# Kernel optimization log

Measured on AMD Instinct MI355X. Metric: run time of the kernel, lower is better.

Reference implementation:

```python
import jax, jax.numpy as jnp
import numpy as np

N = 50000      # nodes
E = 800000     # edges (avg degree 16)
G = 128        # g_dim (input feature dim)
H1 = 128       # h1_dim (RGCN output dim)
H2 = 32        # h2_dim (per-head channels)
HEADS = 4
R = 6          # num_relations
OUT = H2 * HEADS  # 128, BatchNorm width
BN_EPS = 1e-5


def setup_inputs() -> dict:
    key = jax.random.key(0)
    k = jax.random.split(key, 16)
    s = 0.05
    return {
        "node_features": jax.random.normal(k[0], (N, G), jnp.float32),
        "node_type": jax.random.randint(k[1], (N,), 0, 3),
        "edge_index": jax.random.randint(k[2], (2, E), 0, N),
        "edge_type": jax.random.randint(k[3], (E,), 0, R),
        # RGCNConv params (root_weight=True, bias=True, aggr='mean')
        "W_rel": jax.random.normal(k[4], (R, G, H1), jnp.float32) * s,
        "W_root": jax.random.normal(k[5], (G, H1), jnp.float32) * s,
        "b_rgcn": jnp.zeros((H1,), jnp.float32),
        # TransformerConv params (concat=True, root_weight=True via lin_skip)
        "Wq": jax.random.normal(k[6], (H1, OUT), jnp.float32) * s,
        "bq": jnp.zeros((OUT,), jnp.float32),
        "Wk": jax.random.normal(k[7], (H1, OUT), jnp.float32) * s,
        "bk": jnp.zeros((OUT,), jnp.float32),
        "Wv": jax.random.normal(k[8], (H1, OUT), jnp.float32) * s,
        "bv": jnp.zeros((OUT,), jnp.float32),
        "Wskip": jax.random.normal(k[9], (H1, OUT), jnp.float32) * s,
        "bskip": jnp.zeros((OUT,), jnp.float32),
        # BatchNorm1d affine params
        "bn_gamma": jnp.ones((OUT,), jnp.float32),
        "bn_beta": jnp.zeros((OUT,), jnp.float32),
    }


def _gnn_forward(node_features, edge_index, edge_type,
                 W_rel, W_root, b_rgcn,
                 Wq, bq, Wk, bk, Wv, bv, Wskip, bskip,
                 bn_gamma, bn_beta):
    src, dst = edge_index[0], edge_index[1]  # message flows src (j) -> dst (i)

    # ---- RGCNConv with mean aggregation per relation ----
    # Transform all nodes under every relation: [R, N, H1]
    xt = jnp.einsum('nd,rdo->rno', node_features, W_rel)
    msg = xt[edge_type, src]                          # [E, H1]
    seg = edge_type * N + dst                         # composite (relation, dst) segment id
    agg = jax.ops.segment_sum(msg, seg, num_segments=R * N).reshape(R, N, H1)
    cnt = jax.ops.segment_sum(jnp.ones((E,), msg.dtype), seg,
                              num_segments=R * N).reshape(R, N)
    x = node_features @ W_root + b_rgcn + (agg / jnp.maximum(cnt, 1.0)[:, :, None]).sum(0)

    # ---- TransformerConv (heads=HEADS, concat=True) ----
    q = (x @ Wq + bq).reshape(N, HEADS, H2)
    kk = (x @ Wk + bk).reshape(N, HEADS, H2)
    v = (x @ Wv + bv).reshape(N, HEADS, H2)

    score = (q[dst] * kk[src]).sum(-1) / np.sqrt(H2)  # [E, HEADS]
    m = jax.ops.segment_max(score, dst, num_segments=N)   # -inf for isolated nodes
    m = jnp.where(jnp.isfinite(m), m, 0.0)
    ex = jnp.exp(score - m[dst])
    den = jax.ops.segment_sum(ex, dst, num_segments=N)
    alpha = ex / (den[dst] + 1e-16)                   # [E, HEADS]

    out = jax.ops.segment_sum(alpha[:, :, None] * v[src], dst,
                              num_segments=N).reshape(N, OUT)
    out = out + x @ Wskip + bskip                     # skip / root connection

    # ---- BatchNorm1d (training-mode batch stats) + LeakyReLU(0.01) ----
    mu = out.mean(0)
    var = out.var(0)  # biased, as torch uses for normalization
    y = (out - mu) * jax.lax.rsqrt(var + BN_EPS) * bn_gamma + bn_beta
    return jax.nn.leaky_relu(y, negative_slope=0.01)


def reference(node_features, node_type, edge_index, edge_type,
              W_rel, W_root, b_rgcn,
              Wq, bq, Wk, bk, Wv, bv, Wskip, bskip,
              bn_gamma, bn_beta):
    # node_type is accepted but unused, matching the original forward.
    return _gnn_forward(node_features, edge_index, edge_type,
                        W_rel, W_root, b_rgcn,
                        Wq, bq, Wk, bk, Wv, bv, Wskip, bskip,
                        bn_gamma, bn_beta)
```

## Files before the change

### kernel.cpp

```cpp
#include <hip/hip_runtime.h>
#include <hip/hip_fp16.h>
#include <stdint.h>

#define G      128
#define OUTW   128
#define RNUM   6

typedef unsigned short us;
typedef _Float16 f16x8 __attribute__((ext_vector_type(8)));
typedef float    f32x4 __attribute__((ext_vector_type(4)));

__device__ inline float h2f(us u) { __half h; *(us*)&h = u; return __half2float(h); }
__device__ inline us f2h(float f) { __half h = __float2half(f); return *(us*)&h; }

union FragU { f16x8 v; ushort4 u[2]; };

__global__ void count_kernel(const int* __restrict__ ei, const int* __restrict__ et,
                             int* __restrict__ segcnt, int N, int E) {
    int e = blockIdx.x * blockDim.x + threadIdx.x;
    if (e >= E) return;
    int dst = ei[E + e];
    int r   = et[e];
    atomicAdd(&segcnt[dst * RNUM + r], 1);
}

__global__ __launch_bounds__(256)
void scan_part(const int* __restrict__ cnt, int* __restrict__ bsum, int n) {
    __shared__ int s[256];
    int base = blockIdx.x * 1024, t = threadIdx.x;
    int v = 0;
    for (int j = 0; j < 4; ++j) { int idx = base + j * 256 + t; if (idx < n) v += cnt[idx]; }
    s[t] = v; __syncthreads();
    for (int off = 128; off; off >>= 1) { if (t < off) s[t] += s[t + off]; __syncthreads(); }
    if (!t) bsum[blockIdx.x] = s[0];
}

__global__ __launch_bounds__(512)
void scan_top(const int* __restrict__ bsum, int* __restrict__ boff,
              int* __restrict__ segptr, int nb, int n) {
    __shared__ int s[512];
    int t = threadIdx.x;
    int v = (t < nb) ? bsum[t] : 0;
    s[t] = v;
    __syncthreads();
    for (int off = 1; off < 512; off <<= 1) {
        int y = (t >= off) ? s[t - off] : 0;
        __syncthreads();
        s[t] += y;
        __syncthreads();
    }
    if (t < nb) boff[t + 1] = s[t];
    if (!t) boff[0] = 0;
    if (t == nb - 1) segptr[n] = s[t];
}

__global__ __launch_bounds__(256)
void scan_apply(const int* __restrict__ cnt, const int* __restrict__ boff,
                int* __restrict__ segptr, int* __restrict__ cursor, int n) {
    __shared__ int L[1024];
    __shared__ int SS[256];
    int base = blockIdx.x * 1024, t = threadIdx.x;
    for (int j = 0; j < 4; ++j) { int idx = base + j * 256 + t; L[j * 256 + t] = (idx < n) ? cnt[idx] : 0; }
    __syncthreads();
    int s0 = L[t*4] + L[t*4+1] + L[t*4+2] + L[t*4+3];
    SS[t] = s0; __syncthreads();
    for (int off = 1; off < 256; off <<= 1) {
        int y = (t >= off) ? SS[t - off] : 0;
        __syncthreads();
        SS[t] += y;
        __syncthreads();
    }
    int e0 = (t ? SS[t - 1] : 0) + boff[blockIdx.x];
    int4 ov;
    int a;
    a = L[t*4+0]; ov.x = e0; e0 += a;
    a = L[t*4+1]; ov.y = e0; e0 += a;
    a = L[t*4+2]; ov.z = e0; e0 += a;
    a = L[t*4+3]; ov.w = e0; e0 += a;
    int idx0 = base + t * 4;
    if (idx0 + 3 < n) {
        *(int4*)(segptr + idx0) = ov;
        *(int4*)(cursor + idx0) = ov;
    } else {
        int vals[4] = {ov.x, ov.y, ov.z, ov.w};
        for (int k = 0; k < 4; ++k)
            if (idx0 + k < n) { segptr[idx0 + k] = vals[k]; cursor[idx0 + k] = vals[k]; }
    }
}

__global__ void scatter_kernel(const int* __restrict__ ei, const int* __restrict__ et,
                               int* __restrict__ cursor, unsigned* __restrict__ esrc,
                               int N, int E) {
    int e = blockIdx.x * blockDim.x + threadIdx.x;
    if (e >= E) return;
    int src = ei[e];
    int dst = ei[E + e];
    int r   = et[e];
    int pos = atomicAdd(&cursor[dst * RNUM + r], 1);
    esrc[pos] = (unsigned)src;
}

__global__ __launch_bounds__(256)
void prep_kernel(const float* __restrict__ x, us* __restrict__ xh,
                 const float* __restrict__ Wrel, const float* __restrict__ Wroot,
                 ushort4* __restrict__ Btr,
                 const float* __restrict__ Wq, const float* __restrict__ Wk,
                 const float* __restrict__ Wv, const float* __restrict__ Ws,
                 ushort4* __restrict__ Btq, int xblocks) {
    int b = blockIdx.x;
    if (b < xblocks) {
        int i = b * 256 + threadIdx.x;
        float4 a = ((const float4*)x)[2*i];
        float4 c = ((const float4*)x)[2*i+1];
        ushort4 u0 = { f2h(a.x), f2h(a.y), f2h(a.z), f2h(a.w) };
        ushort4 u1 = { f2h(c.x), f2h(c.y), f2h(c.z), f2h(c.w) };
        ((ushort4*)xh)[2*i]   = u0;
        ((ushort4*)xh)[2*i+1] = u1;
    } else if (b < xblocks + 112) {
        int idx = (b - xblocks) * 256 + threadIdx.x;
        int kq = idx >> 7, n = idx & 127;
        ushort4 o;
        us* op = (us*)&o;
#pragma unroll
        for (int i = 0; i < 4; ++i) {
            int k = 4 * kq + i;
            float v = (k < 768) ? Wrel[(size_t)k * 128 + n] : Wroot[(size_t)(k - 768) * 128 + n];
            op[i] = f2h(v);
        }
        Btr[idx] = o;
    } else {
        int idx = (b - xblocks - 112) * 256 + threadIdx.x;
        int kq = idx >> 9, n = idx & 511;
        int quad = n >> 7, nl = n & 127;
        const float* W = (quad == 0) ? Wq : (quad == 1) ? Wk : (quad == 2) ? Wv : Ws;
        ushort4 o;
        us* op = (us*)&o;
#pragma unroll
        for (int i = 0; i < 4; ++i) {
            int k = 4 * kq + i;
            op[i] = f2h(W[(size_t)k * 128 + nl]);
        }
        Btq[idx] = o;
    }
}

__global__ __launch_bounds__(256)
void agg_kernel(const us* __restrict__ xh, const int* __restrict__ segptr,
                const unsigned* __restrict__ esrc, us* __restrict__ meanF, int N) {
    const int wv = threadIdx.x >> 6, l = threadIdx.x & 63;
    const int i = blockIdx.x * 4 + wv;
    if (i >= N) return;
    const int t = i >> 4, row = i & 15;
    const int e0 = __builtin_amdgcn_readfirstlane(segptr[i * RNUM]);
    const int e1 = __builtin_amdgcn_readfirstlane(segptr[i * RNUM + RNUM]);

    int rcur = 0;
    int sstart = e0;
    int bnext = __builtin_amdgcn_readfirstlane(segptr[i * RNUM + 1]);
    float2 a = {0.f, 0.f};
    us* wbase = meanF + (size_t)t * 12288 + row * 4 + (l & 1) * 2;
    const int kqo = (l >> 1) * 64;

#define FLUSH() { \
    float sc_ = 1.f / fmaxf((float)(bnext - sstart), 1.f); \
    ushort2 t2_ = { f2h(a.x * sc_), f2h(a.y * sc_) }; \
    *(ushort2*)(wbase + rcur * 2048 + kqo) = t2_; \
    a.x = 0.f; a.y = 0.f; \
    sstart = bnext; ++rcur; \
    if (rcur < RNUM) bnext = __builtin_amdgcn_readfirstlane(segptr[i * RNUM + rcur + 1]); }

#define GET(J) ((unsigned)__shfl((int)pv, (J)))
#define LX(Q)  (*(const ushort2*)(xh + (size_t)(Q) * G + 2 * l))
#define STEP(U) { while (p >= bnext && rcur < RNUM - 1) FLUSH(); \
                  a.x += h2f((U).x); a.y += h2f((U).y); ++p; }

    int p = e0;
    for (int wb = e0; wb < e1; wb += 64) {
        const int nc = min(64, e1 - wb);
        unsigned pv = (wb + l < e1) ? esrc[wb + l] : 0u;
        int j = 0;
        while (j + 8 <= nc) {
            unsigned q0 = GET(j+0), q1 = GET(j+1), q2 = GET(j+2), q3 = GET(j+3);
            unsigned q4 = GET(j+4), q5 = GET(j+5), q6 = GET(j+6), q7 = GET(j+7);
            ushort2 u0 = LX(q0), u1 = LX(q1), u2 = LX(q2), u3 = LX(q3);
            ushort2 u4 = LX(q4), u5 = LX(q5), u6 = LX(q6), u7 = LX(q7);
            STEP(u0); STEP(u1); STEP(u2); STEP(u3);
            STEP(u4); STEP(u5); STEP(u6); STEP(u7);
            j += 8;
        }
        while (j + 2 <= nc) {
            unsigned q0 = GET(j), q1 = GET(j+1);
            ushort2 u0 = LX(q0), u1 = LX(q1);
            STEP(u0); STEP(u1);
            j += 2;
        }
        if (j < nc) {
            unsigned q0 = GET(j);
            ushort2 u0 = LX(q0);
            STEP(u0);
            ++j;
        }
    }
    while (rcur < RNUM) FLUSH();
#undef STEP
#undef LX
#undef GET
#undef FLUSH
}

__global__ __launch_bounds__(256)
void rgcn_mfma2(const us* __restrict__ xh, const us* __restrict__ meanF,
                const ushort4* __restrict__ Btr, const float* __restrict__ brg,
                us* __restrict__ xrh, int N) {
    const int tid = threadIdx.x;
    const int w = tid >> 6, l = tid & 63;
    const int lh = l >> 4, lm = l & 15;
    const int base = blockIdx.x * 64;
    const int ntile = N >> 4;
    const int t  = min(blockIdx.x * 4 + w, ntile - 1);
    const int gr = min(base + w * 16 + lm, N - 1);
    const us* amean = meanF + (size_t)t * 12288 + lm * 4;
    const us* aroot = xh + (size_t)gr * 128;

    f32x4 acc[8];
#pragma unroll
    for (int ct = 0; ct < 8; ++ct) {
        float b = brg[ct * 16 + lm];
        acc[ct] = (f32x4){b, b, b, b};
    }

#pragma unroll
    for (int s = 0; s < 28; ++s) {
        const int kqg = s * 8 + lh;
        FragU af;
        if (s < 24) {
            af.u[0] = *(const ushort4*)(amean + kqg * 64);
            af.u[1] = *(const ushort4*)(amean + (kqg + 4) * 64);
        } else {
            const int kql = kqg - 192;
            af.u[0] = *(const ushort4*)(aroot + kql * 4);
            af.u[1] = *(const ushort4*)(aroot + kql * 4 + 16);
        }
        const ushort4* B0 = Btr + (size_t)kqg * 128 + lm;
        const ushort4* B1 = B0 + 4 * 128;
#pragma unroll
        for (int ct = 0; ct < 8; ++ct) {
            FragU bf;
            bf.u[0] = B0[ct * 16];
            bf.u[1] = B1[ct * 16];
            acc[ct] = __builtin_amdgcn_mfma_f32_16x16x32_f16(af.v, bf.v, acc[ct], 0, 0, 0);
        }
    }

#pragma unroll
    for (int ct = 0; ct < 8; ++ct) {
#pragma unroll
        for (int i = 0; i < 4; ++i) {
            int r = base + w * 16 + 4 * lh + i;
            if (r < N) xrh[(size_t)r * 128 + ct * 16 + lm] = f2h(acc[ct][i]);
        }
    }
}

__global__ __launch_bounds__(512)
void qkvs_mfma2(const us* __restrict__ xrh, const ushort4* __restrict__ Btq,
                const float* __restrict__ bq, const float* __restrict__ bk,
                const float* __restrict__ bv, const float* __restrict__ bs,
                float* __restrict__ qs, us* __restrict__ kvh, int N) {
    const int tid = threadIdx.x;
    const int w = tid >> 6, l = tid & 63;
    const int quad = w & 3, tp = w >> 2;
    const int lh = l >> 4, lm = l & 15;
    const int base = blockIdx.x * 64;
    const float* bias = (quad == 0) ? bq : (quad == 1) ? bk : (quad == 2) ? bv : bs;

#pragma unroll
    for (int tt = 0; tt < 2; ++tt) {
        const int tile = tp * 2 + tt;
        const int ar = min(base + tile * 16 + lm, N - 1);
        const us* ap = xrh + (size_t)ar * 128;
        f32x4 acc[8];
#pragma unroll
        for (int ct = 0; ct < 8; ++ct) {
            float b = bias[ct * 16 + lm];
            acc[ct] = (f32x4){b, b, b, b};
        }
#pragma unroll
        for (int s = 0; s < 4; ++s) {
            const int kq = s * 8 + lh;
            FragU af;
            af.u[0] = *(const ushort4*)(ap + kq * 4);
            af.u[1] = *(const ushort4*)(ap + kq * 4 + 16);
            const ushort4* B0 = Btq + (size_t)kq * 512 + quad * 128 + lm;
            const ushort4* B1 = B0 + 4 * 512;
#pragma unroll
            for (int ct = 0; ct < 8; ++ct) {
                FragU bf;
                bf.u[0] = B0[ct * 16];
                bf.u[1] = B1[ct * 16];
                acc[ct] = __builtin_amdgcn_mfma_f32_16x16x32_f16(af.v, bf.v, acc[ct], 0, 0, 0);
            }
        }
        if (quad == 0 || quad == 3) {
            int off = (quad == 0) ? 0 : 128;
#pragma unroll
            for (int ct = 0; ct < 8; ++ct)
#pragma unroll
                for (int i = 0; i < 4; ++i) {
                    int r = base + tile * 16 + 4 * lh + i;
                    if (r < N) qs[(size_t)r * 256 + off + ct * 16 + lm] = acc[ct][i];
                }
        } else {
            int off = (quad == 1) ? 0 : 2;
#pragma unroll
            for (int ct = 0; ct < 8; ++ct)
#pragma unroll
                for (int i = 0; i < 4; ++i) {
                    int r = base + tile * 16 + 4 * lh + i;
                    int col = ct * 16 + lm;
                    if (r < N) kvh[(size_t)r * 256 + (col >> 1) * 4 + (col & 1) + off] = f2h(acc[ct][i]);
                }
        }
    }
}

__global__ __launch_bounds__(256)
void attn_kernel(const float* __restrict__ qs, const us* __restrict__ kvh,
                 const int* __restrict__ segptr, const unsigned* __restrict__ esrc,
                 float* __restrict__ out, float* __restrict__ bnS,
                 float* __restrict__ bnQ, int N) {
    __shared__ float sS[128], sQ[128];
    const int tid = threadIdx.x;
    if (tid < 128) { sS[tid] = 0.f; sQ[tid] = 0.f; }
    __syncthreads();

    const int wv = tid >> 6, l = tid & 63;
    const int stride = gridDim.x * 4;
    const float QS = 0.17677669529663687f;
    float2 bsum = {0.f, 0.f}, bsq = {0.f, 0.f};

    for (int i = blockIdx.x * 4 + wv; i < N; i += stride) {
        float2 q2 = *(const float2*)(qs + (size_t)i * 256 + 2*l);
        q2.x *= QS; q2.y *= QS;

        float m = -INFINITY, den = 0.f;
        float2 acc = {0.f, 0.f};
        const int e0 = segptr[(size_t)i * RNUM], e1 = segptr[(size_t)i * RNUM + RNUM];

#define KVLOAD(P) (*(const ushort4*)(kvh + (size_t)(P) * 256 + 4*l))
#define SCORE(U, S) { \
    float s_ = q2.x * h2f((U).x) + q2.y * h2f((U).y); \
    s_ += __shfl_xor(s_, 1, 16); s_ += __shfl_xor(s_, 2, 16); \
    s_ += __shfl_xor(s_, 4, 16); s_ += __shfl_xor(s_, 8, 16); \
    S = s_; }

        for (int base = e0; base < e1; base += 64) {
            const int nc = min(64, e1 - base);
            unsigned pv = 0;
            if (base + l < e1) pv = esrc[base + l];
            int j = 0;
            for (; j + 4 <= nc; j += 4) {
                unsigned p0 = (unsigned)__shfl((int)pv, j+0);
                unsigned p1 = (unsigned)__shfl((int)pv, j+1);
                unsigned p2 = (unsigned)__shfl((int)pv, j+2);
                unsigned p3 = (unsigned)__shfl((int)pv, j+3);
                ushort4 k0 = KVLOAD(p0), k1 = KVLOAD(p1), k2 = KVLOAD(p2), k3 = KVLOAD(p3);
                float s0, s1, s2, s3;
                SCORE(k0, s0); SCORE(k1, s1); SCORE(k2, s2); SCORE(k3, s3);
                float mx = fmaxf(fmaxf(fmaxf(s0, s1), fmaxf(s2, s3)), m);
                float rs = __expf(m - mx);
                float p0e = __expf(s0 - mx), p1e = __expf(s1 - mx);
                float p2e = __expf(s2 - mx), p3e = __expf(s3 - mx);
                den = den * rs + ((p0e + p1e) + (p2e + p3e));
                acc.x = acc.x * rs + p0e*h2f(k0.z) + p1e*h2f(k1.z) + p2e*h2f(k2.z) + p3e*h2f(k3.z);
                acc.y = acc.y * rs + p0e*h2f(k0.w) + p1e*h2f(k1.w) + p2e*h2f(k2.w) + p3e*h2f(k3.w);
                m = mx;
            }
            for (; j < nc; ++j) {
                unsigned p0 = (unsigned)__shfl((int)pv, j);
                ushort4 k0 = KVLOAD(p0);
                float s0; SCORE(k0, s0);
                float mx = fmaxf(m, s0);
                float rs = __expf(m - mx);
                float pe = __expf(s0 - mx);
                den = den * rs + pe;
                acc.x = acc.x * rs + pe * h2f(k0.z);
                acc.y = acc.y * rs + pe * h2f(k0.w);
                m = mx;
            }
        }
#undef SCORE
#undef KVLOAD

        float inv = 1.f / (den + 1e-16f);
        float2 sk = *(const float2*)(qs + (size_t)i * 256 + 128 + 2*l);
        float2 o = { acc.x * inv + sk.x, acc.y * inv + sk.y };
        *(float2*)(out + (size_t)i * OUTW + 2*l) = o;
        bsum.x += o.x; bsum.y += o.y;
        bsq.x  += o.x * o.x; bsq.y += o.y * o.y;
    }

    atomicAdd(&sS[2*l],     bsum.x);
    atomicAdd(&sS[2*l + 1], bsum.y);
    atomicAdd(&sQ[2*l],     bsq.x);
    atomicAdd(&sQ[2*l + 1], bsq.y);
    __syncthreads();
    if (tid < 128) {
        atomicAdd(&bnS[tid], sS[tid]);
        atomicAdd(&bnQ[tid], sQ[tid]);
    }
}

__global__ __launch_bounds__(256)
void apply_kernel(float* __restrict__ out, const float* __restrict__ bnS,
                  const float* __restrict__ bnQ, const float* __restrict__ gamma,
                  const float* __restrict__ beta, int N, int total4) {
    __shared__ float A_s[128], B_s[128];
    const int tid = threadIdx.x;
    if (tid < 128) {
        float fN  = (float)N;
        float mu  = bnS[tid] / fN;
        float var = bnQ[tid] / fN - mu * mu;
        float rv  = rsqrtf(var + 1e-5f);
        float A   = rv * gamma[tid];
        A_s[tid] = A;
        B_s[tid] = beta[tid] - mu * A;
    }
    __syncthreads();
    for (int idx4 = blockIdx.x * 256 + tid; idx4 < total4; idx4 += gridDim.x * 256) {
        float4 v = ((const float4*)out)[idx4];
        int c0 = (idx4 * 4) & 127;
        float y;
        y = A_s[c0    ] * v.x + B_s[c0    ]; v.x = (y > 0.f) ? y : 0.01f * y;
        y = A_s[c0 + 1] * v.y + B_s[c0 + 1]; v.y = (y > 0.f) ? y : 0.01f * y;
        y = A_s[c0 + 2] * v.z + B_s[c0 + 2]; v.z = (y > 0.f) ? y : 0.01f * y;
        y = A_s[c0 + 3] * v.w + B_s[c0 + 3]; v.w = (y > 0.f) ? y : 0.01f * y;
        ((float4*)out)[idx4] = v;
    }
}

static inline char* alignp(char* p) {
    return (char*)(((uintptr_t)p + 255) & ~(uintptr_t)255);
}

extern "C" void kernel_launch(void* const* d_in, const int* in_sizes, int n_in,
                              void* d_out, int out_size, void* d_ws, size_t ws_size,
                              hipStream_t stream) {
    const float* x     = (const float*)d_in[0];
    const int*   ei    = (const int*)  d_in[2];
    const int*   et    = (const int*)  d_in[3];
    const float* Wrel  = (const float*)d_in[4];
    const float* Wroot = (const float*)d_in[5];
    const float* brg   = (const float*)d_in[6];
    const float* Wq    = (const float*)d_in[7];
    const float* bq    = (const float*)d_in[8];
    const float* Wk    = (const float*)d_in[9];
    const float* bk    = (const float*)d_in[10];
    const float* Wv    = (const float*)d_in[11];
    const float* bv    = (const float*)d_in[12];
    const float* Wsk   = (const float*)d_in[13];
    const float* bsk   = (const float*)d_in[14];
    const float* gamma = (const float*)d_in[15];
    const float* beta  = (const float*)d_in[16];
    float* out = (float*)d_out;

    const int N = in_sizes[0] / G;
    const int E = in_sizes[3];
    const int NSEG = N * RNUM;
    const int NB_SCAN = (NSEG + 1023) / 1024;

    char* w = (char*)d_ws;
    int* segcnt = (int*)w;           w += (size_t)NSEG * 4;
    float* bnS = (float*)w;          w += 128 * 4;
    float* bnQ = (float*)w;          w += 128 * 4;
    size_t zero_bytes = (size_t)(w - (char*)d_ws);
    w = alignp(w);
    int* bsum  = (int*)w;            w += 512 * 4;
    int* boff  = (int*)w;            w += 513 * 4;
    w = alignp(w);
    int* segptr = (int*)w;           w += (size_t)(NSEG + 1) * 4;
    w = alignp(w);
    int* cursor = (int*)w;           w += (size_t)NSEG * 4;
    w = alignp(w);
    unsigned* esrc = (unsigned*)w;   w += (size_t)E * 4;
    w = alignp(w);
    us* xh     = (us*)w;             w += (size_t)N * G * 2;
    w = alignp(w);
    us* xrh    = (us*)w;             w += (size_t)N * OUTW * 2;
    w = alignp(w);
    ushort4* Btr = (ushort4*)w;      w += (size_t)224 * 128 * 8;
    w = alignp(w);
    ushort4* Btq = (ushort4*)w;      w += (size_t)32 * 512 * 8;
    w = alignp(w);
    us*    meanF = (us*)w;
    float* qs    = (float*)w;
    us*    kvh   = (us*)(w + (size_t)N * 256 * 4);

    hipMemsetAsync(d_ws, 0, zero_bytes, stream);

    int eb = (E + 255) / 256;
    count_kernel<<<eb, 256, 0, stream>>>(ei, et, segcnt, N, E);

    scan_part<<<NB_SCAN, 256, 0, stream>>>(segcnt, bsum, NSEG);
    scan_top<<<1, 512, 0, stream>>>(bsum, boff, segptr, NB_SCAN, NSEG);
    scan_apply<<<NB_SCAN, 256, 0, stream>>>(segcnt, boff, segptr, cursor, NSEG);

    scatter_kernel<<<eb, 256, 0, stream>>>(ei, et, cursor, esrc, N, E);

    int xblocks = N * G / 8 / 256;
    prep_kernel<<<xblocks + 112 + 64, 256, 0, stream>>>(x, xh, Wrel, Wroot, Btr,
                                                        Wq, Wk, Wv, Wsk, Btq, xblocks);

    agg_kernel<<<(N + 3) / 4, 256, 0, stream>>>(xh, segptr, esrc, meanF, N);

    rgcn_mfma2<<<(N + 63) / 64, 256, 0, stream>>>(xh, meanF, Btr, brg, xrh, N);

    qkvs_mfma2<<<(N + 63) / 64, 512, 0, stream>>>(xrh, Btq, bq, bk, bv, bsk, qs, kvh, N);

    attn_kernel<<<2048, 256, 0, stream>>>(qs, kvh, segptr, esrc, out, bnS, bnQ, N);

    int total4 = N * OUTW / 4;
    apply_kernel<<<2048, 256, 0, stream>>>(out, bnS, bnQ, gamma, beta, N, total4);
}
```

Before: 500.8 us.

## Reuse weight fragments across two row tiles, store Q/skip in fp16, half-wave attention

The RGCN and QKVS MFMA kernels now have each wave compute two 16-row tiles, so every weight fragment loaded from global memory feeds twice as many MFMAs. Q and skip outputs are stored as fp16 instead of fp32, halving that intermediate's traffic and shrinking the workspace. The attention kernel now handles two destination nodes per wave, one per 32-lane half, with 16-byte K/V loads and 4 channels per lane. This raises register pressure and adds fp16 rounding of Q and skip values.

```diff
diff --git a/kernel.cpp b/kernel.cpp
--- a/kernel.cpp
+++ b/kernel.cpp
@@ -12,6 +12,7 @@
 
 __device__ inline float h2f(us u) { __half h; *(us*)&h = u; return __half2float(h); }
 __device__ inline us f2h(float f) { __half h = __float2half(f); return *(us*)&h; }
+__device__ inline float2 h22(int u) { return __half22float2(*(__half2*)&u); }
 
 union FragU { f16x8 v; ushort4 u[2]; };
 
@@ -209,123 +210,156 @@
 }
 
 __global__ __launch_bounds__(256)
-void rgcn_mfma2(const us* __restrict__ xh, const us* __restrict__ meanF,
+void rgcn_mfma3(const us* __restrict__ xh, const us* __restrict__ meanF,
                 const ushort4* __restrict__ Btr, const float* __restrict__ brg,
                 us* __restrict__ xrh, int N) {
     const int tid = threadIdx.x;
     const int w = tid >> 6, l = tid & 63;
     const int lh = l >> 4, lm = l & 15;
-    const int base = blockIdx.x * 64;
+    const int rowbase = blockIdx.x * 128 + w * 32;
     const int ntile = N >> 4;
-    const int t  = min(blockIdx.x * 4 + w, ntile - 1);
-    const int gr = min(base + w * 16 + lm, N - 1);
-    const us* amean = meanF + (size_t)t * 12288 + lm * 4;
-    const us* aroot = xh + (size_t)gr * 128;
-
-    f32x4 acc[8];
-#pragma unroll
-    for (int ct = 0; ct < 8; ++ct) {
-        float b = brg[ct * 16 + lm];
-        acc[ct] = (f32x4){b, b, b, b};
-    }
-
-#pragma unroll
-    for (int s = 0; s < 28; ++s) {
+
+    const us* amean[2];
+    const us* aroot[2];
+#pragma unroll
+    for (int tt = 0; tt < 2; ++tt) {
+        int t  = min((rowbase >> 4) + tt, ntile - 1);
+        int gr = min(rowbase + tt * 16 + lm, N - 1);
+        amean[tt] = meanF + (size_t)t * 12288 + lm * 4;
+        aroot[tt] = xh + (size_t)gr * 128;
+    }
+
+    f32x4 acc[2][8];
+#pragma unroll
+    for (int tt = 0; tt < 2; ++tt)
+#pragma unroll
+        for (int ct = 0; ct < 8; ++ct) {
+            float b = brg[ct * 16 + lm];
+            acc[tt][ct] = (f32x4){b, b, b, b};
+        }
+
+    for (int s = 0; s < 24; ++s) {
         const int kqg = s * 8 + lh;
-        FragU af;
-        if (s < 24) {
-            af.u[0] = *(const ushort4*)(amean + kqg * 64);
-            af.u[1] = *(const ushort4*)(amean + (kqg + 4) * 64);
-        } else {
-            const int kql = kqg - 192;
-            af.u[0] = *(const ushort4*)(aroot + kql * 4);
-            af.u[1] = *(const ushort4*)(aroot + kql * 4 + 16);
-        }
         const ushort4* B0 = Btr + (size_t)kqg * 128 + lm;
         const ushort4* B1 = B0 + 4 * 128;
-#pragma unroll
-        for (int ct = 0; ct < 8; ++ct) {
-            FragU bf;
-            bf.u[0] = B0[ct * 16];
-            bf.u[1] = B1[ct * 16];
-            acc[ct] = __builtin_amdgcn_mfma_f32_16x16x32_f16(af.v, bf.v, acc[ct], 0, 0, 0);
-        }
-    }
-
-#pragma unroll
-    for (int ct = 0; ct < 8; ++ct) {
-#pragma unroll
-        for (int i = 0; i < 4; ++i) {
-            int r = base + w * 16 + 4 * lh + i;
-            if (r < N) xrh[(size_t)r * 128 + ct * 16 + lm] = f2h(acc[ct][i]);
-        }
-    }
-}
-
-__global__ __launch_bounds__(512)
-void qkvs_mfma2(const us* __restrict__ xrh, const ushort4* __restrict__ Btq,
+        FragU bf[8];
+#pragma unroll
+        for (int ct = 0; ct < 8; ++ct) { bf[ct].u[0] = B0[ct * 16]; bf[ct].u[1] = B1[ct * 16]; }
+#pragma unroll
+        for (int tt = 0; tt < 2; ++tt) {
+            FragU af;
+            af.u[0] = *(const ushort4*)(amean[tt] + kqg * 64);
+            af.u[1] = *(const ushort4*)(amean[tt] + (kqg + 4) * 64);
+#pragma unroll
+            for (int ct = 0; ct < 8; ++ct)
+                acc[tt][ct] = __builtin_amdgcn_mfma_f32_16x16x32_f16(af.v, bf[ct].v, acc[tt][ct], 0, 0, 0);
+        }
+    }
+#pragma unroll
+    for (int s = 0; s < 4; ++s) {
+        const int kql = s * 8 + lh;
+        const int kqg = 192 + kql;
+        const ushort4* B0 = Btr + (size_t)kqg * 128 + lm;
+        const ushort4* B1 = B0 + 4 * 128;
+        FragU bf[8];
+#pragma unroll
+        for (int ct = 0; ct < 8; ++ct) { bf[ct].u[0] = B0[ct * 16]; bf[ct].u[1] = B1[ct * 16]; }
+#pragma unroll
+        for (int tt = 0; tt < 2; ++tt) {
+            FragU af;
+            af.u[0] = *(const ushort4*)(aroot[tt] + kql * 4);
+            af.u[1] = *(const ushort4*)(aroot[tt] + kql * 4 + 16);
+#pragma unroll
+            for (int ct = 0; ct < 8; ++ct)
+                acc[tt][ct] = __builtin_amdgcn_mfma_f32_16x16x32_f16(af.v, bf[ct].v, acc[tt][ct], 0, 0, 0);
+        }
+    }
+
+#pragma unroll
+    for (int tt = 0; tt < 2; ++tt)
+#pragma unroll
+        for (int ct = 0; ct < 8; ++ct)
+#pragma unroll
+            for (int i = 0; i < 4; ++i) {
+                int r = rowbase + tt * 16 + 4 * lh + i;
+                if (r < N) xrh[(size_t)r * 128 + ct * 16 + lm] = f2h(acc[tt][ct][i]);
+            }
+}
+
+__global__ __launch_bounds__(256)
+void qkvs_mfma3(const us* __restrict__ xrh, const ushort4* __restrict__ Btq,
                 const float* __restrict__ bq, const float* __restrict__ bk,
                 const float* __restrict__ bv, const float* __restrict__ bs,
-                float* __restrict__ qs, us* __restrict__ kvh, int N) {
+                us* __restrict__ qsh, us* __restrict__ kvh, int N) {
     const int tid = threadIdx.x;
-    const int w = tid >> 6, l = tid & 63;
-    const int quad = w & 3, tp = w >> 2;
+    const int quad = tid >> 6, l = tid & 63;
     const int lh = l >> 4, lm = l & 15;
-    const int base = blockIdx.x * 64;
+    const int base = blockIdx.x * 32;
     const float* bias = (quad == 0) ? bq : (quad == 1) ? bk : (quad == 2) ? bv : bs;
 
+    const us* ap[2];
 #pragma unroll
     for (int tt = 0; tt < 2; ++tt) {
-        const int tile = tp * 2 + tt;
-        const int ar = min(base + tile * 16 + lm, N - 1);
-        const us* ap = xrh + (size_t)ar * 128;
-        f32x4 acc[8];
+        int ar = min(base + tt * 16 + lm, N - 1);
+        ap[tt] = xrh + (size_t)ar * 128;
+    }
+
+    f32x4 acc[2][8];
+#pragma unroll
+    for (int tt = 0; tt < 2; ++tt)
 #pragma unroll
         for (int ct = 0; ct < 8; ++ct) {
             float b = bias[ct * 16 + lm];
-            acc[ct] = (f32x4){b, b, b, b};
-        }
-#pragma unroll
-        for (int s = 0; s < 4; ++s) {
-            const int kq = s * 8 + lh;
+            acc[tt][ct] = (f32x4){b, b, b, b};
+        }
+
+#pragma unroll
+    for (int s = 0; s < 4; ++s) {
+        const int kq = s * 8 + lh;
+        const ushort4* B0 = Btq + (size_t)kq * 512 + quad * 128 + lm;
+        const ushort4* B1 = B0 + 4 * 512;
+        FragU bf[8];
+#pragma unroll
+        for (int ct = 0; ct < 8; ++ct) { bf[ct].u[0] = B0[ct * 16]; bf[ct].u[1] = B1[ct * 16]; }
+#pragma unroll
+        for (int tt = 0; tt < 2; ++tt) {
             FragU af;
-            af.u[0] = *(const ushort4*)(ap + kq * 4);
-            af.u[1] = *(const ushort4*)(ap + kq * 4 + 16);
-            const ushort4* B0 = Btq + (size_t)kq * 512 + quad * 128 + lm;
-            const ushort4* B1 = B0 + 4 * 512;
-#pragma unroll
-            for (int ct = 0; ct < 8; ++ct) {
-                FragU bf;
-                bf.u[0] = B0[ct * 16];
-                bf.u[1] = B1[ct * 16];
-                acc[ct] = __builtin_amdgcn_mfma_f32_16x16x32_f16(af.v, bf.v, acc[ct], 0, 0, 0);
-            }
-        }
-        if (quad == 0 || quad == 3) {
-            int off = (quad == 0) ? 0 : 128;
+            af.u[0] = *(const ushort4*)(ap[tt] + kq * 4);
+            af.u[1] = *(const ushort4*)(ap[tt] + kq * 4 + 16);
 #pragma unroll
             for (int ct = 0; ct < 8; ++ct)
+                acc[tt][ct] = __builtin_amdgcn_mfma_f32_16x16x32_f16(af.v, bf[ct].v, acc[tt][ct], 0, 0, 0);
+        }
+    }
+
+    if (quad == 0 || quad == 3) {
+        const int off = (quad == 0) ? 0 : 128;
+#pragma unroll
+        for (int tt = 0; tt < 2; ++tt)
+#pragma unroll
+            for (int ct = 0; ct < 8; ++ct)
 #pragma unroll
                 for (int i = 0; i < 4; ++i) {
-                    int r = base + tile * 16 + 4 * lh + i;
-                    if (r < N) qs[(size_t)r * 256 + off + ct * 16 + lm] = acc[ct][i];
+                    int r = base + tt * 16 + 4 * lh + i;
+                    if (r < N) qsh[(size_t)r * 256 + off + ct * 16 + lm] = f2h(acc[tt][ct][i]);
                 }
-        } else {
-            int off = (quad == 1) ? 0 : 2;
+    } else {
+        const int off = (quad == 1) ? 0 : 2;
+#pragma unroll
+        for (int tt = 0; tt < 2; ++tt)
 #pragma unroll
             for (int ct = 0; ct < 8; ++ct)
 #pragma unroll
                 for (int i = 0; i < 4; ++i) {
-                    int r = base + tile * 16 + 4 * lh + i;
+                    int r = base + tt * 16 + 4 * lh + i;
                     int col = ct * 16 + lm;
-                    if (r < N) kvh[(size_t)r * 256 + (col >> 1) * 4 + (col & 1) + off] = f2h(acc[ct][i]);
+                    if (r < N) kvh[(size_t)r * 256 + (col >> 1) * 4 + (col & 1) + off] = f2h(acc[tt][ct][i]);
                 }
-        }
-    }
-}
-
-__global__ __launch_bounds__(256)
-void attn_kernel(const float* __restrict__ qs, const us* __restrict__ kvh,
+    }
+}
+
+__global__ __launch_bounds__(256)
+void attn_kernel(const us* __restrict__ qsh, const us* __restrict__ kvh,
                  const int* __restrict__ segptr, const unsigned* __restrict__ esrc,
                  float* __restrict__ out, float* __restrict__ bnS,
                  float* __restrict__ bnQ, int N) {
@@ -335,75 +369,97 @@
     __syncthreads();
 
     const int wv = tid >> 6, l = tid & 63;
-    const int stride = gridDim.x * 4;
+    const int hh = l >> 5, ll = l & 31;
+    const int stride = gridDim.x * 8;
     const float QS = 0.17677669529663687f;
-    float2 bsum = {0.f, 0.f}, bsq = {0.f, 0.f};
-
-    for (int i = blockIdx.x * 4 + wv; i < N; i += stride) {
-        float2 q2 = *(const float2*)(qs + (size_t)i * 256 + 2*l);
-        q2.x *= QS; q2.y *= QS;
+    float4 bsum = {0,0,0,0}, bsq = {0,0,0,0};
+
+#define SCORE(D, S) { \
+    float2 ka_ = h22((D).x), kb_ = h22((D).z); \
+    float t_ = q4.x*ka_.x + q4.y*ka_.y + q4.z*kb_.x + q4.w*kb_.y; \
+    t_ += __shfl_xor(t_, 1, 8); t_ += __shfl_xor(t_, 2, 8); t_ += __shfl_xor(t_, 4, 8); \
+    S = t_; }
+
+    for (int ibase = blockIdx.x * 8 + wv * 2; ibase < N; ibase += stride) {
+        const bool act = (ibase + hh) < N;
+        const int i = min(ibase + hh, N - 1);
+
+        int2 qu = *(const int2*)(qsh + (size_t)i * 256 + 4 * ll);
+        float2 qa = h22(qu.x), qb = h22(qu.y);
+        float4 q4 = { qa.x * QS, qa.y * QS, qb.x * QS, qb.y * QS };
 
         float m = -INFINITY, den = 0.f;
-        float2 acc = {0.f, 0.f};
+        float4 acc = {0,0,0,0};
         const int e0 = segptr[(size_t)i * RNUM], e1 = segptr[(size_t)i * RNUM + RNUM];
 
-#define KVLOAD(P) (*(const ushort4*)(kvh + (size_t)(P) * 256 + 4*l))
-#define SCORE(U, S) { \
-    float s_ = q2.x * h2f((U).x) + q2.y * h2f((U).y); \
-    s_ += __shfl_xor(s_, 1, 16); s_ += __shfl_xor(s_, 2, 16); \
-    s_ += __shfl_xor(s_, 4, 16); s_ += __shfl_xor(s_, 8, 16); \
-    S = s_; }
-
-        for (int base = e0; base < e1; base += 64) {
-            const int nc = min(64, e1 - base);
-            unsigned pv = 0;
-            if (base + l < e1) pv = esrc[base + l];
+        for (int wb = e0; wb < e1; wb += 32) {
+            const int nc = min(32, e1 - wb);
+            unsigned pv = (wb + ll < e1) ? esrc[wb + ll] : 0u;
             int j = 0;
             for (; j + 4 <= nc; j += 4) {
-                unsigned p0 = (unsigned)__shfl((int)pv, j+0);
-                unsigned p1 = (unsigned)__shfl((int)pv, j+1);
-                unsigned p2 = (unsigned)__shfl((int)pv, j+2);
-                unsigned p3 = (unsigned)__shfl((int)pv, j+3);
-                ushort4 k0 = KVLOAD(p0), k1 = KVLOAD(p1), k2 = KVLOAD(p2), k3 = KVLOAD(p3);
+                unsigned p0 = (unsigned)__shfl((int)pv, j+0, 32);
+                unsigned p1 = (unsigned)__shfl((int)pv, j+1, 32);
+                unsigned p2 = (unsigned)__shfl((int)pv, j+2, 32);
+                unsigned p3 = (unsigned)__shfl((int)pv, j+3, 32);
+                int4 d0 = *(const int4*)(kvh + (size_t)p0 * 256 + 8 * ll);
+                int4 d1 = *(const int4*)(kvh + (size_t)p1 * 256 + 8 * ll);
+                int4 d2 = *(const int4*)(kvh + (size_t)p2 * 256 + 8 * ll);
+                int4 d3 = *(const int4*)(kvh + (size_t)p3 * 256 + 8 * ll);
                 float s0, s1, s2, s3;
-                SCORE(k0, s0); SCORE(k1, s1); SCORE(k2, s2); SCORE(k3, s3);
-                float mx = fmaxf(fmaxf(fmaxf(s0, s1), fmaxf(s2, s3)), m);
+                SCORE(d0, s0); SCORE(d1, s1); SCORE(d2, s2); SCORE(d3, s3);
+                float mx = fmaxf(m, fmaxf(fmaxf(s0, s1), fmaxf(s2, s3)));
                 float rs = __expf(m - mx);
-                float p0e = __expf(s0 - mx), p1e = __expf(s1 - mx);
-                float p2e = __expf(s2 - mx), p3e = __expf(s3 - mx);
-                den = den * rs + ((p0e + p1e) + (p2e + p3e));
-                acc.x = acc.x * rs + p0e*h2f(k0.z) + p1e*h2f(k1.z) + p2e*h2f(k2.z) + p3e*h2f(k3.z);
-                acc.y = acc.y * rs + p0e*h2f(k0.w) + p1e*h2f(k1.w) + p2e*h2f(k2.w) + p3e*h2f(k3.w);
+                float w0 = __expf(s0 - mx), w1 = __expf(s1 - mx);
+                float w2 = __expf(s2 - mx), w3 = __expf(s3 - mx);
+                den = den * rs + ((w0 + w1) + (w2 + w3));
+                float2 va0 = h22(d0.y), vb0 = h22(d0.w);
+                float2 va1 = h22(d1.y), vb1 = h22(d1.w);
+                float2 va2 = h22(d2.y), vb2 = h22(d2.w);
+                float2 va3 = h22(d3.y), vb3 = h22(d3.w);
+                acc.x = acc.x * rs + w0*va0.x + w1*va1.x + w2*va2.x + w3*va3.x;
+                acc.y = acc.y * rs + w0*va0.y + w1*va1.y + w2*va2.y + w3*va3.y;
+                acc.z = acc.z * rs + w0*vb0.x + w1*vb1.x + w2*vb2.x + w3*vb3.x;
+                acc.w = acc.w * rs + w0*vb0.y + w1*vb1.y + w2*vb2.y + w3*vb3.y;
                 m = mx;
             }
             for (; j < nc; ++j) {
-                unsigned p0 = (unsigned)__shfl((int)pv, j);
-                ushort4 k0 = KVLOAD(p0);
-                float s0; SCORE(k0, s0);
+                unsigned p0 = (unsigned)__shfl((int)pv, j, 32);
+                int4 d0 = *(const int4*)(kvh + (size_t)p0 * 256 + 8 * ll);
+                float s0; SCORE(d0, s0);
                 float mx = fmaxf(m, s0);
                 float rs = __expf(m - mx);
-                float pe = __expf(s0 - mx);
-                den = den * rs + pe;
-                acc.x = acc.x * rs + pe * h2f(k0.z);
-                acc.y = acc.y * rs + pe * h2f(k0.w);
+                float w0 = __expf(s0 - mx);
+                den = den * rs + w0;
+                float2 va0 = h22(d0.y), vb0 = h22(d0.w);
+                acc.x = acc.x * rs + w0 * va0.x;
+                acc.y = acc.y * rs + w0 * va0.y;
+                acc.z = acc.z * rs + w0 * vb0.x;
+                acc.w = acc.w * rs + w0 * vb0.y;
                 m = mx;
             }
         }
+
+        float inv = 1.f / (den + 1e-16f);
+        int2 su = *(const int2*)(qsh + (size_t)i * 256 + 128 + 4 * ll);
+        float2 sa = h22(su.x), sb = h22(su.y);
+        float4 o = { acc.x * inv + sa.x, acc.y * inv + sa.y,
+                     acc.z * inv + sb.x, acc.w * inv + sb.y };
+        if (act) {
+            *(float4*)(out + (size_t)i * OUTW + 4 * ll) = o;
+            bsum.x += o.x; bsum.y += o.y; bsum.z += o.z; bsum.w += o.w;
+            bsq.x += o.x*o.x; bsq.y += o.y*o.y; bsq.z += o.z*o.z; bsq.w += o.w*o.w;
+        }
+    }
 #undef SCORE
-#undef KVLOAD
-
-        float inv = 1.f / (den + 1e-16f);
-        float2 sk = *(const float2*)(qs + (size_t)i * 256 + 128 + 2*l);
-        float2 o = { acc.x * inv + sk.x, acc.y * inv + sk.y };
-        *(float2*)(out + (size_t)i * OUTW + 2*l) = o;
-        bsum.x += o.x; bsum.y += o.y;
-        bsq.x  += o.x * o.x; bsq.y += o.y * o.y;
-    }
-
-    atomicAdd(&sS[2*l],     bsum.x);
-    atomicAdd(&sS[2*l + 1], bsum.y);
-    atomicAdd(&sQ[2*l],     bsq.x);
-    atomicAdd(&sQ[2*l + 1], bsq.y);
+
+    atomicAdd(&sS[4*ll + 0], bsum.x);
+    atomicAdd(&sS[4*ll + 1], bsum.y);
+    atomicAdd(&sS[4*ll + 2], bsum.z);
+    atomicAdd(&sS[4*ll + 3], bsum.w);
+    atomicAdd(&sQ[4*ll + 0], bsq.x);
+    atomicAdd(&sQ[4*ll + 1], bsq.y);
+    atomicAdd(&sQ[4*ll + 2], bsq.z);
+    atomicAdd(&sQ[4*ll + 3], bsq.w);
     __syncthreads();
     if (tid < 128) {
         atomicAdd(&bnS[tid], sS[tid]);
@@ -492,9 +548,9 @@
     w = alignp(w);
     ushort4* Btq = (ushort4*)w;      w += (size_t)32 * 512 * 8;
     w = alignp(w);
-    us*    meanF = (us*)w;
-    float* qs    = (float*)w;
-    us*    kvh   = (us*)(w + (size_t)N * 256 * 4);
+    us* meanF = (us*)w;
+    us* qsh   = (us*)w;
+    us* kvh   = (us*)(w + (size_t)N * 256 * 2);
 
     hipMemsetAsync(d_ws, 0, zero_bytes, stream);
 
@@ -513,11 +569,11 @@
 
     agg_kernel<<<(N + 3) / 4, 256, 0, stream>>>(xh, segptr, esrc, meanF, N);
 
-    rgcn_mfma2<<<(N + 63) / 64, 256, 0, stream>>>(xh, meanF, Btr, brg, xrh, N);
-
-    qkvs_mfma2<<<(N + 63) / 64, 512, 0, stream>>>(xrh, Btq, bq, bk, bv, bsk, qs, kvh, N);
-
-    attn_kernel<<<2048, 256, 0, stream>>>(qs, kvh, segptr, esrc, out, bnS, bnQ, N);
+    rgcn_mfma3<<<(N + 127) / 128, 256, 0, stream>>>(xh, meanF, Btr, brg, xrh, N);
+
+    qkvs_mfma3<<<(N + 31) / 32, 256, 0, stream>>>(xrh, Btq, bq, bk, bv, bsk, qsh, kvh, N);
+
+    attn_kernel<<<2048, 256, 0, stream>>>(qsh, kvh, segptr, esrc, out, bnS, bnQ, N);
 
     int total4 = N * OUTW / 4;
     apply_kernel<<<2048, 256, 0, stream>>>(out, bnS, bnQ, gamma, beta, N, total4);
```

After: 453.9 us. 9.4% less time.
